# Kernel optimization log

Hardware: AMD Instinct MI355X
Metric: run time of the kernel (lower is better)

## Reference

```python
import jax, jax.numpy as jnp
import numpy as np

N = 262144          # total points
C = 16              # classes
AVG_DEG = 16
E = N * AVG_DEG     # edges
LAMBDA1 = 0.7
LAMBDA2 = 0.5
LAMBDA_S = 0.2
LOSS_WEIGHT = 1.0
IGNORE_INDEX = -1
EPS = 1e-8


def setup_inputs() -> dict:
    key = jax.random.key(0)
    k1, k2, k3, k4 = jax.random.split(key, 4)
    pred = jax.random.normal(k1, (N, C), dtype=jnp.float32)
    target = jax.random.randint(k2, (N,), 0, C, dtype=jnp.int64)
    # precomputed radius-graph edge list (row = destination, col = source)
    row = jax.random.randint(k3, (E,), 0, N, dtype=jnp.int64)
    col = jax.random.randint(k4, (E,), 0, N, dtype=jnp.int64)
    return {"pred": pred, "target": target, "row": row, "col": col}


def _masked_mean(x, mask):
    cnt = jnp.sum(mask.astype(x.dtype))
    s = jnp.sum(jnp.where(mask, x, jnp.zeros_like(x)))
    return jnp.where(cnt > 0, s / jnp.maximum(cnt, 1.0), s)


def reference(pred, target, row, col):
    # per-point CE (reduction='none'); ignored points contribute 0
    log_probs = jax.nn.log_softmax(pred, axis=1)          # [N, C]
    probs = jnp.exp(log_probs)                            # [N, C]
    valid_mask = target != IGNORE_INDEX
    tgt = jnp.where(valid_mask, target, 0)
    ce_per_point = -jnp.take_along_axis(log_probs, tgt[:, None], axis=1)[:, 0]
    ce_per_point = jnp.where(valid_mask, ce_per_point, 0.0)

    conf = jnp.max(probs, axis=1)                         # [N]
    pred_label = jnp.argmax(probs, axis=1)                # [N]

    # degree per destination node
    deg = jax.ops.segment_sum(jnp.ones((E,), dtype=probs.dtype), row, num_segments=N)

    # neighborhood agreement u_i = mean_{j in N(i)} [pred_j == pred_i]
    agree_edge = (pred_label[col] == pred_label[row]).astype(probs.dtype)
    sum_agree = jax.ops.segment_sum(agree_edge, row, num_segments=N)
    u = jnp.where(deg > 0, sum_agree / jnp.maximum(deg, 1.0), jnp.ones_like(sum_agree))

    w = 1.0 + LAMBDA1 * (1.0 - u) + LAMBDA2 * (1.0 - conf)
    loss_ce = _masked_mean(w * ce_per_point, valid_mask)

    # per-edge KL(p_i || p_j) with clamp at 1e-8, scatter-mean over neighbors
    pi = probs[row]                                       # [E, C]
    pj = probs[col]                                       # [E, C]
    kl_edge = jnp.sum(
        pi * (jnp.log(jnp.maximum(pi, EPS)) - jnp.log(jnp.maximum(pj, EPS))), axis=1
    )                                                     # [E]
    sum_kl = jax.ops.segment_sum(kl_edge, row, num_segments=N)
    mean_kl = jnp.where(deg > 0, sum_kl / jnp.maximum(deg, 1.0), jnp.zeros_like(sum_kl))
    loss_smooth = _masked_mean(mean_kl, valid_mask)

    return (loss_ce + LAMBDA_S * loss_smooth) * LOSS_WEIGHT
```

## Files before the change

kernel.cpp:

```cpp
#include <hip/hip_runtime.h>

constexpr float LAMBDA1  = 0.7f;
constexpr float LAMBDA2  = 0.5f;
constexpr float LAMBDA_S = 0.2f;
constexpr float LOG_EPS  = -18.420680743952367f;
constexpr float PQ_SCALE  = 15.0f;
constexpr float LQ_SCALE4 = 15.0f / 18.420680743952367f;
constexpr float DOT_SCALE4 = 18.420680743952367f / (15.0f * 15.0f);

constexpr int      BUCK_SHIFT = 10;
constexpr unsigned BUCK_CAP   = 20480u;
constexpr int      CHUNK      = 8192;
constexpr int      FT         = 1024;
constexpr int      RT         = 1024;
constexpr int      CUR_PAD    = 16;

#if defined(__has_builtin)
#if __has_builtin(__builtin_amdgcn_udot8)
#define HAS_UDOT8 1
#endif
#endif

__global__ void __launch_bounds__(FT, 8)
k_fused(const float* __restrict__ pred,
        const int*   __restrict__ target,
        unsigned long long* __restrict__ probsQ4,
        unsigned long long* __restrict__ logpQ4,
        float* __restrict__ Hn,
        float* __restrict__ confn,
        float* __restrict__ cen,
        const int* __restrict__ row,
        const int* __restrict__ col,
        unsigned* __restrict__ bucketed,
        unsigned* __restrict__ gcursor,
        int n, int e, int bucketBlocks) {
    int t = threadIdx.x;

    if ((int)blockIdx.x < bucketBlocks) {
        __shared__ unsigned stage[CHUNK];
        __shared__ unsigned char bid[CHUNK];
        __shared__ unsigned hist[256];
        __shared__ unsigned cnt[256];
        __shared__ unsigned lofs[256];
        __shared__ unsigned baseArr[256];

        if (t < 256) { hist[t] = 0; cnt[t] = 0; }
        __syncthreads();

        long i0 = (long)blockIdx.x * CHUNK;
        int chunkN = (int)(((long)e - i0) < CHUNK ? ((long)e - i0) : CHUNK);
        if (chunkN < 0) chunkN = 0;

        for (int k = t; k < chunkN; k += FT) {
            int r = __builtin_nontemporal_load(row + i0 + k);
            atomicAdd(&hist[r >> BUCK_SHIFT], 1u);
        }
        __syncthreads();

        if (t < 64) {
            unsigned h0 = hist[4 * t], h1 = hist[4 * t + 1],
                     h2 = hist[4 * t + 2], h3 = hist[4 * t + 3];
            unsigned s = h0 + h1 + h2 + h3;
            unsigned inc = s;
#pragma unroll
            for (int off = 1; off < 64; off <<= 1) {
                unsigned v = __shfl_up(inc, off, 64);
                if (t >= off) inc += v;
            }
            unsigned run = inc - s;
            lofs[4 * t]     = run;
            lofs[4 * t + 1] = run + h0;
            lofs[4 * t + 2] = run + h0 + h1;
            lofs[4 * t + 3] = run + h0 + h1 + h2;
#pragma unroll
            for (int j = 0; j < 4; ++j) {
                int b = 4 * t + j;
                unsigned h = hist[b];
                baseArr[b] = (unsigned)b * BUCK_CAP
                           + atomicAdd(&gcursor[b * CUR_PAD], h);
            }
        }
        __syncthreads();

        for (int k = t; k < chunkN; k += FT) {
            int r = row[i0 + k];
            int c = __builtin_nontemporal_load(col + i0 + k);
            int b = r >> BUCK_SHIFT;
            unsigned s = lofs[b] + atomicAdd(&cnt[b], 1u);
            stage[s] = ((unsigned)(r & 1023) << 18) | (unsigned)c;
            bid[s]   = (unsigned char)b;
        }
        __syncthreads();

        for (int k = t; k < chunkN; k += FT) {
            unsigned b   = bid[k];
            unsigned dst = baseArr[b] + ((unsigned)k - lofs[b]);
            if (dst < (b + 1) * BUCK_CAP)
                bucketed[dst] = stage[k];
        }
    } else {
        int i = (blockIdx.x - bucketBlocks) * FT + t;
        if (i >= n) return;

        const float4* p4 = reinterpret_cast<const float4*>(pred + (size_t)i * 16);
        float4 v0 = p4[0], v1 = p4[1], v2 = p4[2], v3 = p4[3];
        float x[16] = {v0.x, v0.y, v0.z, v0.w,
                       v1.x, v1.y, v1.z, v1.w,
                       v2.x, v2.y, v2.z, v2.w,
                       v3.x, v3.y, v3.z, v3.w};

        float m = x[0];
#pragma unroll
        for (int c = 1; c < 16; ++c) m = fmaxf(m, x[c]);

        float s = 0.f;
#pragma unroll
        for (int c = 0; c < 16; ++c) s += __expf(x[c] - m);
        float logZ = m + __logf(s);

        unsigned long long pq64 = 0ull, lq64 = 0ull;
        float Hacc = 0.f;
#pragma unroll
        for (int c = 0; c < 16; ++c) {
            float lp  = x[c] - logZ;
            float p   = __expf(lp);
            float lpc = fmaxf(lp, LOG_EPS);
            Hacc += p * lpc;

            unsigned pq = (unsigned)(int)rintf(p * PQ_SCALE);
            unsigned lq = (unsigned)(int)rintf(-lpc * LQ_SCALE4);
            pq64 |= (unsigned long long)pq << (4 * c);
            lq64 |= (unsigned long long)lq << (4 * c);
        }

        probsQ4[i] = pq64;
        logpQ4[i]  = lq64;

        Hn[i]    = Hacc;
        confn[i] = __expf(m - logZ);

        int tt0 = target[i];
        bool valid = (tt0 != -1);
        int tt = valid ? tt0 : 0;
        float xt = x[0];
#pragma unroll
        for (int c = 1; c < 16; ++c) xt = (c == tt) ? x[c] : xt;
        cen[i] = valid ? -(xt - logZ) : 0.f;
    }
}

__global__ void __launch_bounds__(RT)
k_reduce(const unsigned* __restrict__ bucketed,
         const unsigned* __restrict__ gcursor,
         const unsigned long long* __restrict__ probsQ4,
         const unsigned long long* __restrict__ logpQ4,
         const int*   __restrict__ target,
         const float* __restrict__ confn,
         const float* __restrict__ cen,
         const float* __restrict__ Hn,
         float* __restrict__ partial,
         int n) {
    __shared__ unsigned long long acc[1024];
    __shared__ unsigned long long Ptab[1024];
    __shared__ unsigned char labr[1024];
    __shared__ float sred[3][16];
    int t = threadIdx.x;
    int b = blockIdx.x;

    {
        acc[t] = 0ull;
        int node = (b << BUCK_SHIFT) + t;
        unsigned long long P = (node < n) ? probsQ4[node] : 0ull;
        Ptab[t] = P;
        unsigned plo = (unsigned)P, phi = (unsigned)(P >> 32);
        int lr = 0, mr = -1;
#pragma unroll
        for (int k2 = 0; k2 < 8; ++k2) {
            int pv = (int)((plo >> (4 * k2)) & 15u);
            if (pv > mr) { mr = pv; lr = k2; }
        }
#pragma unroll
        for (int k2 = 0; k2 < 8; ++k2) {
            int pv = (int)((phi >> (4 * k2)) & 15u);
            if (pv > mr) { mr = pv; lr = 8 + k2; }
        }
        labr[t] = (unsigned char)lr;
    }
    __syncthreads();

    unsigned nb = gcursor[b * CUR_PAD];
    if (nb > BUCK_CAP) nb = BUCK_CAP;
    unsigned base = (unsigned)b * BUCK_CAP;

    for (unsigned k = (unsigned)t; k < nb; k += RT) {
        unsigned pl = bucketed[base + k];
        unsigned c  = pl & 0x3FFFFu;
        unsigned lr = pl >> 18;
        unsigned long long P = Ptab[lr];
        unsigned long long L = logpQ4[c];
        unsigned plo = (unsigned)P, phi = (unsigned)(P >> 32);
        unsigned llo = (unsigned)L, lhi = (unsigned)(L >> 32);

        unsigned dot;
#ifdef HAS_UDOT8
        dot = __builtin_amdgcn_udot8(plo, llo, 0u, false);
        dot = __builtin_amdgcn_udot8(phi, lhi, dot, false);
#else
        dot = 0;
#pragma unroll
        for (int k2 = 0; k2 < 8; ++k2) {
            dot += ((plo >> (4 * k2)) & 15u) * ((llo >> (4 * k2)) & 15u);
            dot += ((phi >> (4 * k2)) & 15u) * ((lhi >> (4 * k2)) & 15u);
        }
#endif
        int lab_c = 0, mc = 1000;
#pragma unroll
        for (int k2 = 0; k2 < 8; ++k2) {
            int lv = (int)((llo >> (4 * k2)) & 15u);
            if (lv < mc) { mc = lv; lab_c = k2; }
        }
#pragma unroll
        for (int k2 = 0; k2 < 8; ++k2) {
            int lv = (int)((lhi >> (4 * k2)) & 15u);
            if (lv < mc) { mc = lv; lab_c = 8 + k2; }
        }

        unsigned agree = ((int)labr[lr] == lab_c) ? 1u : 0u;
        unsigned long long add =
            ((unsigned long long)(0x10000u | agree) << 32)
            | (unsigned long long)dot;
        atomicAdd(&acc[lr], add);
    }
    __syncthreads();

    float wce = 0.f, mkl = 0.f, v = 0.f;
    {
        int node = (b << BUCK_SHIFT) + t;
        if (node < n) {
            unsigned long long pk = acc[t];
            float deg  = (float)(unsigned)(pk >> 48);
            float sag  = (float)(unsigned)((pk >> 32) & 0xFFFFu);
            float sdot = (float)(unsigned)(pk & 0xFFFFFFFFull);
            float u  = (deg > 0.f) ? sag / deg : 1.f;
            float mk = (deg > 0.f) ? (Hn[node] + sdot * DOT_SCALE4 / deg) : 0.f;
            float w  = 1.f + LAMBDA1 * (1.f - u) + LAMBDA2 * (1.f - confn[node]);
            int tg = target[node];
            if (tg != -1) {
                wce = w * cen[node];
                mkl = mk;
                v   = 1.f;
            }
        }
    }
#pragma unroll
    for (int off = 32; off > 0; off >>= 1) {
        wce += __shfl_down(wce, off, 64);
        mkl += __shfl_down(mkl, off, 64);
        v   += __shfl_down(v,   off, 64);
    }
    int wave = t >> 6, lane = t & 63;
    if (lane == 0) { sred[0][wave] = wce; sred[1][wave] = mkl; sred[2][wave] = v; }
    __syncthreads();
    if (t < 16) {
        float a = sred[0][t], bb = sred[1][t], c = sred[2][t];
#pragma unroll
        for (int off = 8; off > 0; off >>= 1) {
            a  += __shfl_down(a,  off, 64);
            bb += __shfl_down(bb, off, 64);
            c  += __shfl_down(c,  off, 64);
        }
        if (t == 0) {
            float4* p4 = reinterpret_cast<float4*>(partial);
            p4[b] = make_float4(a, bb, c, 0.f);
        }
    }
}

__global__ void k_final(const float* __restrict__ partial, float* __restrict__ out) {
    int t = threadIdx.x;
    const float4* p4 = reinterpret_cast<const float4*>(partial);
    float4 pv = p4[t];
    float wce = pv.x, mkl = pv.y, v = pv.z;
#pragma unroll
    for (int off = 32; off > 0; off >>= 1) {
        wce += __shfl_down(wce, off, 64);
        mkl += __shfl_down(mkl, off, 64);
        v   += __shfl_down(v,   off, 64);
    }
    __shared__ float s[3][4];
    int wave = t >> 6, lane = t & 63;
    if (lane == 0) { s[0][wave] = wce; s[1][wave] = mkl; s[2][wave] = v; }
    __syncthreads();
    if (t == 0) {
        float a = 0.f, b = 0.f, c = 0.f;
#pragma unroll
        for (int w = 0; w < 4; ++w) { a += s[0][w]; b += s[1][w]; c += s[2][w]; }
        float lce = (c > 0.f) ? a / fmaxf(c, 1.f) : a;
        float ls  = (c > 0.f) ? b / fmaxf(c, 1.f) : b;
        out[0] = lce + LAMBDA_S * ls;
    }
}

extern "C" void kernel_launch(void* const* d_in, const int* in_sizes, int n_in,
                              void* d_out, int out_size, void* d_ws, size_t ws_size,
                              hipStream_t stream) {
    const float* pred   = (const float*)d_in[0];
    const int*   target = (const int*)d_in[1];
    const int*   row    = (const int*)d_in[2];
    const int*   col    = (const int*)d_in[3];
    float* out = (float*)d_out;

    const int n = in_sizes[1];
    const int e = in_sizes[2];

    const int nbuck = (n + 1023) >> BUCK_SHIFT;
    const int bucketBlocks = (e + CHUNK - 1) / CHUNK;
    const int pointBlocks  = (n + FT - 1) / FT;

    char* base = (char*)d_ws;
    size_t off = 0;
    unsigned long long* probsQ4 = (unsigned long long*)(base + off); off += (size_t)n * 8;
    unsigned long long* logpQ4  = (unsigned long long*)(base + off); off += (size_t)n * 8;
    float* Hn     = (float*)(base + off); off += (size_t)n * sizeof(float);
    float* confn  = (float*)(base + off); off += (size_t)n * sizeof(float);
    float* cen    = (float*)(base + off); off += (size_t)n * sizeof(float);
    unsigned* bucketed = (unsigned*)(base + off); off += (size_t)nbuck * BUCK_CAP * 4;
    unsigned* gcursor  = (unsigned*)(base + off); off += (size_t)nbuck * CUR_PAD * 4;
    float* partial = (float*)(base + off); off += (size_t)nbuck * 4 * sizeof(float);

    hipMemsetAsync(gcursor, 0, (size_t)nbuck * CUR_PAD * 4, stream);

    k_fused<<<bucketBlocks + pointBlocks, FT, 0, stream>>>(
        pred, target, probsQ4, logpQ4, Hn, confn, cen,
        row, col, bucketed, gcursor, n, e, bucketBlocks);
    k_reduce<<<nbuck, RT, 0, stream>>>(bucketed, gcursor, probsQ4, logpQ4,
                                       target, confn, cen, Hn, partial, n);
    k_final<<<1, 256, 0, stream>>>(partial, out);
}
```

Baseline: 142.2 us.

## Halve bucket size to 512 nodes and keep edge loads in registers

Each bucket now covers 512 nodes instead of 1024, giving 512 buckets. This doubles the number of reduce blocks, so more of the GPU is used, and it shrinks per-bucket capacity and shared tables. The binning pass now loads row and col once into registers (8 per thread) and reuses them in the scatter phase, instead of re-reading row from global memory. In exchange it uses more registers, 16-bit bucket ids, a wider scan, and reduce blocks where only 512 of 1024 threads own nodes. k_final widens to 512 threads to match.

```diff
diff --git a/kernel.cpp b/kernel.cpp
--- a/kernel.cpp
+++ b/kernel.cpp
@@ -8,10 +8,11 @@
 constexpr float LQ_SCALE4 = 15.0f / 18.420680743952367f;
 constexpr float DOT_SCALE4 = 18.420680743952367f / (15.0f * 15.0f);
 
-constexpr int      BUCK_SHIFT = 10;
-constexpr unsigned BUCK_CAP   = 20480u;
+constexpr int      BUCK_SHIFT = 9;
+constexpr unsigned BUCK_CAP   = 10240u;
 constexpr int      CHUNK      = 8192;
 constexpr int      FT         = 1024;
+constexpr int      EPT        = CHUNK / FT;
 constexpr int      RT         = 1024;
 constexpr int      CUR_PAD    = 16;
 
@@ -38,57 +39,61 @@
 
     if ((int)blockIdx.x < bucketBlocks) {
         __shared__ unsigned stage[CHUNK];
-        __shared__ unsigned char bid[CHUNK];
-        __shared__ unsigned hist[256];
-        __shared__ unsigned cnt[256];
-        __shared__ unsigned lofs[256];
-        __shared__ unsigned baseArr[256];
-
-        if (t < 256) { hist[t] = 0; cnt[t] = 0; }
+        __shared__ unsigned short bid[CHUNK];
+        __shared__ unsigned hist[512];
+        __shared__ unsigned cnt[512];
+        __shared__ unsigned lofs[512];
+        __shared__ unsigned baseArr[512];
+
+        if (t < 512) { hist[t] = 0; cnt[t] = 0; }
         __syncthreads();
 
         long i0 = (long)blockIdx.x * CHUNK;
         int chunkN = (int)(((long)e - i0) < CHUNK ? ((long)e - i0) : CHUNK);
         if (chunkN < 0) chunkN = 0;
 
-        for (int k = t; k < chunkN; k += FT) {
-            int r = __builtin_nontemporal_load(row + i0 + k);
-            atomicAdd(&hist[r >> BUCK_SHIFT], 1u);
+        int rr[EPT], cc[EPT];
+#pragma unroll
+        for (int j = 0; j < EPT; ++j) {
+            int k = t + j * FT;
+            if (k < chunkN) {
+                rr[j] = __builtin_nontemporal_load(row + i0 + k);
+                cc[j] = __builtin_nontemporal_load(col + i0 + k);
+                atomicAdd(&hist[rr[j] >> BUCK_SHIFT], 1u);
+            }
         }
         __syncthreads();
 
         if (t < 64) {
-            unsigned h0 = hist[4 * t], h1 = hist[4 * t + 1],
-                     h2 = hist[4 * t + 2], h3 = hist[4 * t + 3];
-            unsigned s = h0 + h1 + h2 + h3;
+            unsigned h[8], s = 0;
+#pragma unroll
+            for (int j = 0; j < 8; ++j) { h[j] = hist[8 * t + j]; s += h[j]; }
             unsigned inc = s;
 #pragma unroll
             for (int off = 1; off < 64; off <<= 1) {
                 unsigned v = __shfl_up(inc, off, 64);
                 if (t >= off) inc += v;
             }
-            unsigned run = inc - s;
-            lofs[4 * t]     = run;
-            lofs[4 * t + 1] = run + h0;
-            lofs[4 * t + 2] = run + h0 + h1;
-            lofs[4 * t + 3] = run + h0 + h1 + h2;
-#pragma unroll
-            for (int j = 0; j < 4; ++j) {
-                int b = 4 * t + j;
-                unsigned h = hist[b];
+            unsigned pre = inc - s;
+#pragma unroll
+            for (int j = 0; j < 8; ++j) {
+                int b = 8 * t + j;
+                lofs[b] = pre; pre += h[j];
                 baseArr[b] = (unsigned)b * BUCK_CAP
-                           + atomicAdd(&gcursor[b * CUR_PAD], h);
+                           + atomicAdd(&gcursor[b * CUR_PAD], h[j]);
             }
         }
         __syncthreads();
 
-        for (int k = t; k < chunkN; k += FT) {
-            int r = row[i0 + k];
-            int c = __builtin_nontemporal_load(col + i0 + k);
-            int b = r >> BUCK_SHIFT;
-            unsigned s = lofs[b] + atomicAdd(&cnt[b], 1u);
-            stage[s] = ((unsigned)(r & 1023) << 18) | (unsigned)c;
-            bid[s]   = (unsigned char)b;
+#pragma unroll
+        for (int j = 0; j < EPT; ++j) {
+            int k = t + j * FT;
+            if (k < chunkN) {
+                int b = rr[j] >> BUCK_SHIFT;
+                unsigned s = lofs[b] + atomicAdd(&cnt[b], 1u);
+                stage[s] = ((unsigned)(rr[j] & 511) << 18) | (unsigned)cc[j];
+                bid[s]   = (unsigned short)b;
+            }
         }
         __syncthreads();
 
@@ -149,7 +154,7 @@
     }
 }
 
-__global__ void __launch_bounds__(RT)
+__global__ void __launch_bounds__(RT, 8)
 k_reduce(const unsigned* __restrict__ bucketed,
          const unsigned* __restrict__ gcursor,
          const unsigned long long* __restrict__ probsQ4,
@@ -160,14 +165,14 @@
          const float* __restrict__ Hn,
          float* __restrict__ partial,
          int n) {
-    __shared__ unsigned long long acc[1024];
-    __shared__ unsigned long long Ptab[1024];
-    __shared__ unsigned char labr[1024];
+    __shared__ unsigned long long acc[512];
+    __shared__ unsigned long long Ptab[512];
+    __shared__ unsigned char labr[512];
     __shared__ float sred[3][16];
     int t = threadIdx.x;
     int b = blockIdx.x;
 
-    {
+    if (t < 512) {
         acc[t] = 0ull;
         int node = (b << BUCK_SHIFT) + t;
         unsigned long long P = (node < n) ? probsQ4[node] : 0ull;
@@ -234,7 +239,7 @@
     __syncthreads();
 
     float wce = 0.f, mkl = 0.f, v = 0.f;
-    {
+    if (t < 512) {
         int node = (b << BUCK_SHIFT) + t;
         if (node < n) {
             unsigned long long pk = acc[t];
@@ -287,14 +292,14 @@
         mkl += __shfl_down(mkl, off, 64);
         v   += __shfl_down(v,   off, 64);
     }
-    __shared__ float s[3][4];
+    __shared__ float s[3][8];
     int wave = t >> 6, lane = t & 63;
     if (lane == 0) { s[0][wave] = wce; s[1][wave] = mkl; s[2][wave] = v; }
     __syncthreads();
     if (t == 0) {
         float a = 0.f, b = 0.f, c = 0.f;
 #pragma unroll
-        for (int w = 0; w < 4; ++w) { a += s[0][w]; b += s[1][w]; c += s[2][w]; }
+        for (int w = 0; w < 8; ++w) { a += s[0][w]; b += s[1][w]; c += s[2][w]; }
         float lce = (c > 0.f) ? a / fmaxf(c, 1.f) : a;
         float ls  = (c > 0.f) ? b / fmaxf(c, 1.f) : b;
         out[0] = lce + LAMBDA_S * ls;
@@ -313,7 +318,7 @@
     const int n = in_sizes[1];
     const int e = in_sizes[2];
 
-    const int nbuck = (n + 1023) >> BUCK_SHIFT;
+    const int nbuck = (n + 511) >> BUCK_SHIFT;
     const int bucketBlocks = (e + CHUNK - 1) / CHUNK;
     const int pointBlocks  = (n + FT - 1) / FT;
 
@@ -335,5 +340,5 @@
         row, col, bucketed, gcursor, n, e, bucketBlocks);
     k_reduce<<<nbuck, RT, 0, stream>>>(bucketed, gcursor, probsQ4, logpQ4,
                                        target, confn, cen, Hn, partial, n);
-    k_final<<<1, 256, 0, stream>>>(partial, out);
+    k_final<<<1, 512, 0, stream>>>(partial, out);
 }
```

Result: no change. 145.0 us (+2.0%).
